# Optimization experiments

Hardware: AMD Instinct MI355X
Metric: run time of the kernel (lower is better)

Reference implementation:

```python
import jax, jax.numpy as jnp
import numpy as np

DIM = 768
N_HEADS = 12
HEAD_DIM = DIM // N_HEADS
MLP_DIM = 3072
DEPTH = 12
B, N = 16, 512


def setup_inputs() -> dict:
    key = jax.random.key(0)
    ks = jax.random.split(key, 12)
    s = 0.02
    return {
        "x": jax.random.normal(ks[0], (B, N, DIM), dtype=jnp.float32),
        "ln_w": jnp.ones((DIM,), jnp.float32),
        "ln_b": jnp.zeros((DIM,), jnp.float32),
        "wq": jax.random.normal(ks[1], (DIM, DIM), jnp.float32) * s,
        "bq": jnp.zeros((DIM,), jnp.float32),
        "wk": jax.random.normal(ks[2], (DIM, DIM), jnp.float32) * s,
        "bk": jnp.zeros((DIM,), jnp.float32),
        "wv": jax.random.normal(ks[3], (DIM, DIM), jnp.float32) * s,
        "bv": jnp.zeros((DIM,), jnp.float32),
        "w1": jax.random.normal(ks[4], (DIM, MLP_DIM), jnp.float32) * s,
        "b1": jnp.zeros((MLP_DIM,), jnp.float32),
        "w2": jax.random.normal(ks[5], (MLP_DIM, DIM), jnp.float32) * s,
        "b2": jnp.zeros((DIM,), jnp.float32),
    }


def _layernorm(x, w, b):
    mu = jnp.mean(x, axis=-1, keepdims=True)
    var = jnp.var(x, axis=-1, keepdims=True)
    return (x - mu) * jax.lax.rsqrt(var + 1e-5) * w + b


def _mha(x, wq, bq, wk, bk, wv, bv):
    # x: [b, n, dim]; weights stored as [in, out]
    def heads(t):
        return t.reshape(B, N, N_HEADS, HEAD_DIM).transpose(0, 2, 1, 3)  # b h n d
    q = heads(x @ wq + bq)
    k = heads(x @ wk + bk)
    v = heads(x @ wv + bv)
    scores = jnp.einsum('bhqd,bhkd->bhqk', q, k) / np.sqrt(HEAD_DIM).astype(np.float32)
    attn = jax.nn.softmax(scores, axis=-1)
    o = jnp.einsum('bhqk,bhkd->bhqd', attn, v)
    return o.transpose(0, 2, 1, 3).reshape(B, N, DIM)


def reference(x, ln_w, ln_b, wq, bq, wk, bk, wv, bv, w1, b1, w2, b2):
    # Dropout is identity in eval mode. Same weights reused each depth iteration.
    for _ in range(DEPTH):
        x = _mha(_layernorm(x, ln_w, ln_b), wq, bq, wk, bk, wv, bv) + x
        h = _layernorm(x, ln_w, ln_b)
        h = jax.nn.gelu(h @ w1 + b1, approximate=False) @ w2 + b2
        x = h + x
    return x
```

## Files before the change

### kernel.cpp

```cpp
#include <hip/hip_runtime.h>

typedef __bf16 bf16x8 __attribute__((ext_vector_type(8)));
typedef float f32x4 __attribute__((ext_vector_type(4)));
typedef unsigned short ushort8_t __attribute__((ext_vector_type(8)));
typedef unsigned short ushort4_t __attribute__((ext_vector_type(4)));

#define MFMA16(a, b, c) __builtin_amdgcn_mfma_f32_16x16x32_bf16((a), (b), (c), 0, 0, 0)

#define GLOAD16(gp, lp)                                                        \
  __builtin_amdgcn_global_load_lds(                                            \
      (__attribute__((address_space(1))) void*)(gp),                           \
      (__attribute__((address_space(3))) void*)(lp), 16, 0, 0)

__device__ __forceinline__ unsigned short f2bf(float f) {
  unsigned u = __builtin_bit_cast(unsigned, f);
  return (unsigned short)((u + 0x7FFFu + ((u >> 16) & 1u)) >> 16);
}

__global__ __launch_bounds__(256) void transpose_f2b(
    const float* __restrict__ src, unsigned short* __restrict__ dst,
    int Kdim, int Ndim) {
  long i = (long)blockIdx.x * 256 + threadIdx.x;
  if (i >= (long)Kdim * Ndim) return;
  int n = (int)(i / Kdim);
  int kk = (int)(i - (long)n * Kdim);
  dst[i] = f2bf(src[(long)kk * Ndim + n]);
}

__global__ __launch_bounds__(256) void ln_kernel(
    const float* __restrict__ x, const float* __restrict__ gw,
    const float* __restrict__ gb, unsigned short* __restrict__ h) {
  const int row = blockIdx.x * 4 + (threadIdx.x >> 6);
  const int l = threadIdx.x & 63;
  const float* xr = x + (long)row * 768;
  f32x4 va[3];
#pragma unroll
  for (int i = 0; i < 3; i++) va[i] = *(const f32x4*)(xr + i * 256 + l * 4);
  float s = 0.f, ss = 0.f;
#pragma unroll
  for (int i = 0; i < 3; i++)
#pragma unroll
    for (int j = 0; j < 4; j++) {
      float t = va[i][j];
      s += t;
      ss += t * t;
    }
#pragma unroll
  for (int off = 1; off < 64; off <<= 1) {
    s += __shfl_xor(s, off, 64);
    ss += __shfl_xor(ss, off, 64);
  }
  const float mu = s * (1.f / 768.f);
  const float var = ss * (1.f / 768.f) - mu * mu;
  const float inv = rsqrtf(var + 1e-5f);
  unsigned short* hp = h + (long)row * 768;
#pragma unroll
  for (int i = 0; i < 3; i++) {
    f32x4 wv = *(const f32x4*)(gw + i * 256 + l * 4);
    f32x4 bv = *(const f32x4*)(gb + i * 256 + l * 4);
    ushort4_t o;
#pragma unroll
    for (int j = 0; j < 4; j++) o[j] = f2bf((va[i][j] - mu) * inv * wv[j] + bv[j]);
    *(ushort4_t*)(hp + i * 256 + l * 4) = o;
  }
}

__global__ __launch_bounds__(256) void transpose_v(
    const unsigned short* __restrict__ v, unsigned short* __restrict__ vt) {
  __shared__ unsigned short t[64 * 65];
  const int n0 = blockIdx.x * 64;
  const int bh = blockIdx.y;
  const int tid = threadIdx.x;
  {
    const int n = tid >> 2, d0 = (tid & 3) * 16;
    const unsigned short* s = v + ((long)bh * 512 + n0 + n) * 64 + d0;
    ushort8_t r0 = *(const ushort8_t*)s;
    ushort8_t r1 = *(const ushort8_t*)(s + 8);
#pragma unroll
    for (int j = 0; j < 8; j++) {
      t[n * 65 + d0 + j] = r0[j];
      t[n * 65 + d0 + 8 + j] = r1[j];
    }
  }
  __syncthreads();
  {
    const int d = tid >> 2, nb = (tid & 3) * 16;
    ushort8_t r0, r1;
#pragma unroll
    for (int j = 0; j < 8; j++) {
      r0[j] = t[(nb + j) * 65 + d];
      r1[j] = t[(nb + 8 + j) * 65 + d];
    }
    unsigned short* o = vt + ((long)bh * 64 + d) * 512 + n0 + nb;
    *(ushort8_t*)o = r0;
    *(ushort8_t*)(o + 8) = r1;
  }
}

enum { EPI_QKV = 0, EPI_GELU = 1, EPI_RES = 2 };

template <int EPI, int MREP>
__global__ __launch_bounds__(256) void gemm_bt(
    const unsigned short* __restrict__ A, const unsigned short* __restrict__ BT,
    int K, const float* __restrict__ bb0, const float* __restrict__ bb1,
    const float* __restrict__ bb2, unsigned short* __restrict__ o0,
    unsigned short* __restrict__ o1, unsigned short* __restrict__ o2,
    float* oF) {
  constexpr int BM = MREP * 32;
  constexpr int ABUF = BM * 32;
  __shared__ unsigned short As[2][ABUF];
  __shared__ unsigned short Bs[2][128 * 32];
  const int tid = threadIdx.x;
  const int w = tid >> 6, l = tid & 63;
  const int lr = l & 15, lg = l >> 4;
  const int wr = w >> 1, wc = w & 1;

  const int nx = gridDim.x;
  const int nwg = nx * gridDim.y;
  int wg = blockIdx.y * nx + blockIdx.x;
  {
    const int qq = nwg >> 3, rr = nwg & 7;
    const int xcd = wg & 7, idx = wg >> 3;
    wg = (xcd < rr ? xcd * (qq + 1) : rr * (qq + 1) + (xcd - rr) * qq) + idx;
  }
  const int bx = wg % nx, by = wg / nx;
  const int m0 = by * BM, n0 = bx * 128;

  const unsigned short* Ag =
      A + (long)(m0 + w * (BM / 4) + (l >> 2)) * K + (l & 3) * 8;
  const unsigned short* Bg = BT + (long)(n0 + w * 32 + (l >> 2)) * K + (l & 3) * 8;
  unsigned short* AsW = &As[0][w * (BM / 4) * 32 + l * 8];
  unsigned short* BsW = &Bs[0][w * 1024 + l * 8];

  auto stage = [&](int buf, int kt) {
    const unsigned short* ag = Ag + kt * 32;
    const unsigned short* bg = Bg + kt * 32;
    unsigned short* aw = AsW + buf * ABUF;
    unsigned short* bw = BsW + buf * 4096;
#pragma unroll
    for (int i = 0; i < BM / 64; i++) GLOAD16(ag + i * 16 * K, aw + i * 512);
    GLOAD16(bg, bw);
    GLOAD16(bg + 16 * K, bw + 512);
  };

  f32x4 acc[MREP][4] = {};
  const int nk = K >> 5;
  stage(0, 0);
  __syncthreads();
  for (int kt = 0; kt < nk; ++kt) {
    const int cur = kt & 1;
    if (kt + 1 < nk) stage(cur ^ 1, kt + 1);
    const unsigned short* Ab = &As[cur][0];
    const unsigned short* Bb = &Bs[cur][0];
    bf16x8 a[MREP], b[4];
#pragma unroll
    for (int i = 0; i < MREP; i++)
      a[i] = *(const bf16x8*)(Ab + (wr * MREP * 16 + i * 16 + lr) * 32 + lg * 8);
#pragma unroll
    for (int j = 0; j < 4; j++)
      b[j] = *(const bf16x8*)(Bb + (wc * 64 + j * 16 + lr) * 32 + lg * 8);
#pragma unroll
    for (int i = 0; i < MREP; i++)
#pragma unroll
      for (int j = 0; j < 4; j++) acc[i][j] = MFMA16(a[i], b[j], acc[i][j]);
    __syncthreads();
  }

  if (EPI == EPI_QKV) {
    const int whichq = n0 / 768;
    const int cc0 = n0 - whichq * 768;
    const float* bias = whichq == 0 ? bb0 : whichq == 1 ? bb1 : bb2;
    unsigned short* dst = whichq == 0 ? o0 : whichq == 1 ? o1 : o2;
#pragma unroll
    for (int i = 0; i < MREP; i++) {
      const int r = m0 + wr * MREP * 16 + i * 16 + lg * 4;
#pragma unroll
      for (int j = 0; j < 4; j++) {
        const int ccol = cc0 + wc * 64 + j * 16 + lr;
        const int hd = ccol >> 6, d = ccol & 63;
        const float bv = bias[ccol];
#pragma unroll
        for (int q = 0; q < 4; q++) {
          const int row = r + q;
          const int bidx = row >> 9, n = row & 511;
          const long addr = ((long)(bidx * 12 + hd) * 512 + n) * 64 + d;
          dst[addr] = f2bf(acc[i][j][q] + bv);
        }
      }
    }
  } else if (EPI == EPI_GELU) {
#pragma unroll
    for (int i = 0; i < MREP; i++) {
      const int r = m0 + wr * MREP * 16 + i * 16 + lg * 4;
#pragma unroll
      for (int j = 0; j < 4; j++) {
        const int c = n0 + wc * 64 + j * 16 + lr;
        const float bv = bb0[c];
#pragma unroll
        for (int q = 0; q < 4; q++) {
          float v = acc[i][j][q] + bv;
          const float u = v * (0.7978845608f + 0.0356774081f * v * v);
          const float g = v / (1.0f + __expf(-2.0f * u));
          o0[(long)(r + q) * 3072 + c] = f2bf(g);
        }
      }
    }
  } else {
#pragma unroll
    for (int i = 0; i < MREP; i++) {
      const int r = m0 + wr * MREP * 16 + i * 16 + lg * 4;
#pragma unroll
      for (int j = 0; j < 4; j++) {
        const int c = n0 + wc * 64 + j * 16 + lr;
        const float bv = bb0[c];
#pragma unroll
        for (int q = 0; q < 4; q++) {
          const long addr = (long)(r + q) * 768 + c;
          oF[addr] = acc[i][j][q] + bv + oF[addr];
        }
      }
    }
  }
}

__global__ __launch_bounds__(256) void attn_kernel(
    const unsigned short* __restrict__ qg, const unsigned short* __restrict__ kg,
    const unsigned short* __restrict__ vtg, float* __restrict__ x) {
  __shared__ unsigned short Qs[128 * 64];
  __shared__ unsigned short Ks[2][64 * 64];
  __shared__ unsigned short Vt[2][64 * 64];
  __shared__ unsigned short Ps[4][32 * 64];
  const int qt = blockIdx.x, h = blockIdx.y, b = blockIdx.z;
  const int bh = b * 12 + h;
  const int tid = threadIdx.x, w = tid >> 6, l = tid & 63;
  const int lr = l & 15, lg = l >> 4;

  const unsigned short* qrow =
      qg + ((long)bh * 512 + qt * 128 + w * 32 + (l >> 3)) * 64 + (l & 7) * 8;
  unsigned short* QsW = &Qs[w * 2048 + l * 8];
#pragma unroll
  for (int cc = 0; cc < 4; cc++) GLOAD16(qrow + cc * 8 * 64, QsW + cc * 512);

  const unsigned short* krow =
      kg + ((long)bh * 512 + w * 16 + (l >> 3)) * 64 + (l & 7) * 8;
  const unsigned short* vrow =
      vtg + ((long)bh * 64 + w * 16 + (l >> 3)) * 512 + (l & 7) * 8;
  unsigned short* KsW = &Ks[0][w * 1024 + l * 8];
  unsigned short* VtW = &Vt[0][w * 1024 + l * 8];
  unsigned short* Pw = &Ps[w][0];

  auto stageKV = [&](int buf, int kt) {
#pragma unroll
    for (int cc = 0; cc < 2; cc++) {
      GLOAD16(krow + (kt * 64 + cc * 8) * 64, KsW + buf * 4096 + cc * 512);
      GLOAD16(vrow + cc * 8 * 512 + kt * 64, VtW + buf * 4096 + cc * 512);
    }
  };
  stageKV(0, 0);
  __syncthreads();

  bf16x8 qa[2][2];
#pragma unroll
  for (int mi = 0; mi < 2; mi++)
#pragma unroll
    for (int ds = 0; ds < 2; ds++) {
      qa[mi][ds] =
          *(const bf16x8*)(Qs + (w * 32 + mi * 16 + lr) * 64 + ds * 32 + lg * 8);
#pragma unroll
      for (int e = 0; e < 8; e++)
        qa[mi][ds][e] = (__bf16)(0.125f * (float)qa[mi][ds][e]);
    }

  float lsum[8] = {};
  f32x4 o[2][4] = {};

  for (int kt = 0; kt < 8; ++kt) {
    const int cur = kt & 1;
    if (kt < 7) stageKV(cur ^ 1, kt + 1);

    f32x4 s[2][4] = {};
#pragma unroll
    for (int ds = 0; ds < 2; ++ds) {
      bf16x8 kb[4];
#pragma unroll
      for (int nj = 0; nj < 4; nj++)
        kb[nj] = *(const bf16x8*)(&Ks[cur][0] + (nj * 16 + lr) * 64 + ds * 32 + lg * 8);
#pragma unroll
      for (int mi = 0; mi < 2; mi++)
#pragma unroll
        for (int nj = 0; nj < 4; nj++) s[mi][nj] = MFMA16(qa[mi][ds], kb[nj], s[mi][nj]);
    }

#pragma unroll
    for (int mi = 0; mi < 2; mi++)
#pragma unroll
      for (int nj = 0; nj < 4; nj++)
#pragma unroll
        for (int q = 0; q < 4; q++) {
          const float p = __expf(s[mi][nj][q]);
          lsum[mi * 4 + q] += p;
          Pw[(mi * 16 + lg * 4 + q) * 64 + nj * 16 + lr] = f2bf(p);
        }

#pragma unroll
    for (int ks = 0; ks < 2; ++ks) {
      bf16x8 pa[2], vb[4];
#pragma unroll
      for (int mi = 0; mi < 2; mi++)
        pa[mi] = *(const bf16x8*)(Pw + (mi * 16 + lr) * 64 + ks * 32 + lg * 8);
#pragma unroll
      for (int dj = 0; dj < 4; dj++)
        vb[dj] = *(const bf16x8*)(&Vt[cur][0] + (dj * 16 + lr) * 64 + ks * 32 + lg * 8);
#pragma unroll
      for (int mi = 0; mi < 2; mi++)
#pragma unroll
        for (int dj = 0; dj < 4; dj++) o[mi][dj] = MFMA16(pa[mi], vb[dj], o[mi][dj]);
    }
    __syncthreads();
  }

#pragma unroll
  for (int i = 0; i < 8; i++) {
#pragma unroll
    for (int off = 1; off < 16; off <<= 1) lsum[i] += __shfl_xor(lsum[i], off, 64);
  }

#pragma unroll
  for (int mi = 0; mi < 2; mi++) {
#pragma unroll
    for (int q = 0; q < 4; q++) {
      const int n = qt * 128 + w * 32 + mi * 16 + lg * 4 + q;
      const float inv = 1.0f / lsum[mi * 4 + q];
      const long base = ((long)(b * 512 + n)) * 768 + h * 64;
#pragma unroll
      for (int dj = 0; dj < 4; dj++) {
        const long a = base + dj * 16 + lr;
        x[a] = x[a] + o[mi][dj][q] * inv;
      }
    }
  }
}

extern "C" void kernel_launch(void* const* d_in, const int* in_sizes, int n_in,
                              void* d_out, int out_size, void* d_ws,
                              size_t ws_size, hipStream_t stream) {
  const float* x_in = (const float*)d_in[0];
  const float* ln_w = (const float*)d_in[1];
  const float* ln_b = (const float*)d_in[2];
  const float* wq = (const float*)d_in[3];
  const float* bq = (const float*)d_in[4];
  const float* wk = (const float*)d_in[5];
  const float* bk = (const float*)d_in[6];
  const float* wv = (const float*)d_in[7];
  const float* bv = (const float*)d_in[8];
  const float* w1 = (const float*)d_in[9];
  const float* b1 = (const float*)d_in[10];
  const float* w2 = (const float*)d_in[11];
  const float* b2 = (const float*)d_in[12];

  char* p = (char*)d_ws;
  float* xw = (float*)p;            p += 8192L * 768 * 4;
  unsigned short* hbuf = (unsigned short*)p;  p += 8192L * 768 * 2;
  unsigned short* wqkvT = (unsigned short*)p; p += 2304L * 768 * 2;
  unsigned short* w1T = (unsigned short*)p;   p += 3072L * 768 * 2;
  unsigned short* w2T = (unsigned short*)p;   p += 768L * 3072 * 2;
  unsigned short* qb = (unsigned short*)p;
  unsigned short* kb = qb + 6291456L;
  unsigned short* vb = kb + 6291456L;
  unsigned short* vt = vb + 6291456L;
  unsigned short* gbuf = qb;

  hipMemcpyAsync(xw, x_in, 8192L * 768 * 4, hipMemcpyDeviceToDevice, stream);

  transpose_f2b<<<(768 * 768 + 255) / 256, 256, 0, stream>>>(wq, wqkvT, 768, 768);
  transpose_f2b<<<(768 * 768 + 255) / 256, 256, 0, stream>>>(wk, wqkvT + 589824L, 768, 768);
  transpose_f2b<<<(768 * 768 + 255) / 256, 256, 0, stream>>>(wv, wqkvT + 1179648L, 768, 768);
  transpose_f2b<<<(768 * 3072 + 255) / 256, 256, 0, stream>>>(w1, w1T, 768, 3072);
  transpose_f2b<<<(768 * 3072 + 255) / 256, 256, 0, stream>>>(w2, w2T, 3072, 768);

  for (int layer = 0; layer < 12; ++layer) {
    ln_kernel<<<2048, 256, 0, stream>>>(xw, ln_w, ln_b, hbuf);
    gemm_bt<EPI_QKV, 4><<<dim3(18, 64), 256, 0, stream>>>(
        hbuf, wqkvT, 768, bq, bk, bv, qb, kb, vb, nullptr);
    transpose_v<<<dim3(8, 192), 256, 0, stream>>>(vb, vt);
    attn_kernel<<<dim3(4, 12, 16), 256, 0, stream>>>(qb, kb, vt, xw);
    ln_kernel<<<2048, 256, 0, stream>>>(xw, ln_w, ln_b, hbuf);
    gemm_bt<EPI_GELU, 4><<<dim3(24, 64), 256, 0, stream>>>(
        hbuf, w1T, 768, b1, nullptr, nullptr, gbuf, nullptr, nullptr, nullptr);
    gemm_bt<EPI_RES, 2><<<dim3(6, 128), 256, 0, stream>>>(
        gbuf, w2T, 3072, b2, nullptr, nullptr, nullptr, nullptr, nullptr, xw);
  }

  hipMemcpyAsync(d_out, xw, 8192L * 768 * 4, hipMemcpyDeviceToDevice, stream);
}
```

Baseline: 2.856 ms.

## Swizzle LDS tiles, write V transposed in QKV epilogue, drop final copy

Applies an XOR swizzle to the global-to-LDS chunk placement and the matching fragment reads in both the GEMM and attention kernels, to remove LDS bank conflicts. The QKV GEMM epilogue now writes V directly in transposed layout, which removes the separate transpose_v kernel and its extra read and write of V. Attention reuses the Q shared buffer for the P tile, cutting LDS usage and possibly raising occupancy. The last MLP residual GEMM writes straight to the output, which removes the final device-to-device copy. The swizzle indexing must match exactly between the load and read sides, and the transposed V stores are 8-byte scattered writes.

```diff
diff --git a/kernel.cpp b/kernel.cpp
--- a/kernel.cpp
+++ b/kernel.cpp
@@ -65,38 +65,6 @@
   }
 }
 
-__global__ __launch_bounds__(256) void transpose_v(
-    const unsigned short* __restrict__ v, unsigned short* __restrict__ vt) {
-  __shared__ unsigned short t[64 * 65];
-  const int n0 = blockIdx.x * 64;
-  const int bh = blockIdx.y;
-  const int tid = threadIdx.x;
-  {
-    const int n = tid >> 2, d0 = (tid & 3) * 16;
-    const unsigned short* s = v + ((long)bh * 512 + n0 + n) * 64 + d0;
-    ushort8_t r0 = *(const ushort8_t*)s;
-    ushort8_t r1 = *(const ushort8_t*)(s + 8);
-#pragma unroll
-    for (int j = 0; j < 8; j++) {
-      t[n * 65 + d0 + j] = r0[j];
-      t[n * 65 + d0 + 8 + j] = r1[j];
-    }
-  }
-  __syncthreads();
-  {
-    const int d = tid >> 2, nb = (tid & 3) * 16;
-    ushort8_t r0, r1;
-#pragma unroll
-    for (int j = 0; j < 8; j++) {
-      r0[j] = t[(nb + j) * 65 + d];
-      r1[j] = t[(nb + 8 + j) * 65 + d];
-    }
-    unsigned short* o = vt + ((long)bh * 64 + d) * 512 + n0 + nb;
-    *(ushort8_t*)o = r0;
-    *(ushort8_t*)(o + 8) = r1;
-  }
-}
-
 enum { EPI_QKV = 0, EPI_GELU = 1, EPI_RES = 2 };
 
 template <int EPI, int MREP>
@@ -105,7 +73,7 @@
     int K, const float* __restrict__ bb0, const float* __restrict__ bb1,
     const float* __restrict__ bb2, unsigned short* __restrict__ o0,
     unsigned short* __restrict__ o1, unsigned short* __restrict__ o2,
-    float* oF) {
+    const float* oFin, float* oFout) {
   constexpr int BM = MREP * 32;
   constexpr int ABUF = BM * 32;
   __shared__ unsigned short As[2][ABUF];
@@ -114,6 +82,8 @@
   const int w = tid >> 6, l = tid & 63;
   const int lr = l & 15, lg = l >> 4;
   const int wr = w >> 1, wc = w & 1;
+  const int fchunk = ((l & 3) ^ ((l >> 3) & 3)) * 8;
+  const int sR = (lr >> 1) & 3;
 
   const int nx = gridDim.x;
   const int nwg = nx * gridDim.y;
@@ -127,8 +97,8 @@
   const int m0 = by * BM, n0 = bx * 128;
 
   const unsigned short* Ag =
-      A + (long)(m0 + w * (BM / 4) + (l >> 2)) * K + (l & 3) * 8;
-  const unsigned short* Bg = BT + (long)(n0 + w * 32 + (l >> 2)) * K + (l & 3) * 8;
+      A + (long)(m0 + w * (BM / 4) + (l >> 2)) * K + fchunk;
+  const unsigned short* Bg = BT + (long)(n0 + w * 32 + (l >> 2)) * K + fchunk;
   unsigned short* AsW = &As[0][w * (BM / 4) * 32 + l * 8];
   unsigned short* BsW = &Bs[0][w * 1024 + l * 8];
 
@@ -150,15 +120,15 @@
   for (int kt = 0; kt < nk; ++kt) {
     const int cur = kt & 1;
     if (kt + 1 < nk) stage(cur ^ 1, kt + 1);
-    const unsigned short* Ab = &As[cur][0];
-    const unsigned short* Bb = &Bs[cur][0];
     bf16x8 a[MREP], b[4];
 #pragma unroll
     for (int i = 0; i < MREP; i++)
-      a[i] = *(const bf16x8*)(Ab + (wr * MREP * 16 + i * 16 + lr) * 32 + lg * 8);
+      a[i] = *(const bf16x8*)(&As[cur][(wr * MREP * 16 + i * 16 + lr) * 32 +
+                                       ((lg ^ sR) * 8)]);
 #pragma unroll
     for (int j = 0; j < 4; j++)
-      b[j] = *(const bf16x8*)(Bb + (wc * 64 + j * 16 + lr) * 32 + lg * 8);
+      b[j] = *(const bf16x8*)(&Bs[cur][(wc * 64 + j * 16 + lr) * 32 +
+                                       ((lg ^ sR) * 8)]);
 #pragma unroll
     for (int i = 0; i < MREP; i++)
 #pragma unroll
@@ -170,21 +140,39 @@
     const int whichq = n0 / 768;
     const int cc0 = n0 - whichq * 768;
     const float* bias = whichq == 0 ? bb0 : whichq == 1 ? bb1 : bb2;
-    unsigned short* dst = whichq == 0 ? o0 : whichq == 1 ? o1 : o2;
-#pragma unroll
-    for (int i = 0; i < MREP; i++) {
-      const int r = m0 + wr * MREP * 16 + i * 16 + lg * 4;
-#pragma unroll
-      for (int j = 0; j < 4; j++) {
-        const int ccol = cc0 + wc * 64 + j * 16 + lr;
-        const int hd = ccol >> 6, d = ccol & 63;
-        const float bv = bias[ccol];
-#pragma unroll
-        for (int q = 0; q < 4; q++) {
-          const int row = r + q;
-          const int bidx = row >> 9, n = row & 511;
-          const long addr = ((long)(bidx * 12 + hd) * 512 + n) * 64 + d;
-          dst[addr] = f2bf(acc[i][j][q] + bv);
+    if (whichq < 2) {
+      unsigned short* dst = whichq == 0 ? o0 : o1;
+#pragma unroll
+      for (int i = 0; i < MREP; i++) {
+        const int r = m0 + wr * MREP * 16 + i * 16 + lg * 4;
+#pragma unroll
+        for (int j = 0; j < 4; j++) {
+          const int ccol = cc0 + wc * 64 + j * 16 + lr;
+          const int hd = ccol >> 6, d = ccol & 63;
+          const float bv = bias[ccol];
+#pragma unroll
+          for (int q = 0; q < 4; q++) {
+            const int row = r + q;
+            const int bidx = row >> 9, n = row & 511;
+            const long addr = ((long)(bidx * 12 + hd) * 512 + n) * 64 + d;
+            dst[addr] = f2bf(acc[i][j][q] + bv);
+          }
+        }
+      }
+    } else {
+#pragma unroll
+      for (int i = 0; i < MREP; i++) {
+        const int r = m0 + wr * MREP * 16 + i * 16 + lg * 4;
+        const int bidx = r >> 9, n = r & 511;
+#pragma unroll
+        for (int j = 0; j < 4; j++) {
+          const int ccol = cc0 + wc * 64 + j * 16 + lr;
+          const int hd = ccol >> 6, d = ccol & 63;
+          const float bv = bias[ccol];
+          ushort4_t pk;
+#pragma unroll
+          for (int q = 0; q < 4; q++) pk[q] = f2bf(acc[i][j][q] + bv);
+          *(ushort4_t*)(&o2[((long)(bidx * 12 + hd) * 64 + d) * 512 + n]) = pk;
         }
       }
     }
@@ -216,7 +204,7 @@
 #pragma unroll
         for (int q = 0; q < 4; q++) {
           const long addr = (long)(r + q) * 768 + c;
-          oF[addr] = acc[i][j][q] + bv + oF[addr];
+          oFout[addr] = acc[i][j][q] + bv + oFin[addr];
         }
       }
     }
@@ -226,34 +214,34 @@
 __global__ __launch_bounds__(256) void attn_kernel(
     const unsigned short* __restrict__ qg, const unsigned short* __restrict__ kg,
     const unsigned short* __restrict__ vtg, float* __restrict__ x) {
-  __shared__ unsigned short Qs[128 * 64];
+  __shared__ unsigned short Sh[128 * 64];
   __shared__ unsigned short Ks[2][64 * 64];
   __shared__ unsigned short Vt[2][64 * 64];
-  __shared__ unsigned short Ps[4][32 * 64];
   const int qt = blockIdx.x, h = blockIdx.y, b = blockIdx.z;
   const int bh = b * 12 + h;
   const int tid = threadIdx.x, w = tid >> 6, l = tid & 63;
   const int lr = l & 15, lg = l >> 4;
-
-  const unsigned short* qrow =
-      qg + ((long)bh * 512 + qt * 128 + w * 32 + (l >> 3)) * 64 + (l & 7) * 8;
-  unsigned short* QsW = &Qs[w * 2048 + l * 8];
-#pragma unroll
-  for (int cc = 0; cc < 4; cc++) GLOAD16(qrow + cc * 8 * 64, QsW + cc * 512);
-
-  const unsigned short* krow =
-      kg + ((long)bh * 512 + w * 16 + (l >> 3)) * 64 + (l & 7) * 8;
-  const unsigned short* vrow =
-      vtg + ((long)bh * 64 + w * 16 + (l >> 3)) * 512 + (l & 7) * 8;
+  const int fchunk = ((l & 7) ^ ((l >> 3) & 7)) * 8;
+  const int rk = lr & 7;
+
+  const unsigned short* qbase =
+      qg + ((long)bh * 512 + qt * 128 + w * 32 + (l >> 3)) * 64 + fchunk;
+  unsigned short* shW = &Sh[w * 2048 + l * 8];
+#pragma unroll
+  for (int cc = 0; cc < 4; cc++) GLOAD16(qbase + cc * 8 * 64, shW + cc * 512);
+
+  const unsigned short* kbase =
+      kg + ((long)bh * 512 + w * 16 + (l >> 3)) * 64 + fchunk;
+  const unsigned short* vbase =
+      vtg + ((long)bh * 64 + w * 16 + (l >> 3)) * 512 + fchunk;
   unsigned short* KsW = &Ks[0][w * 1024 + l * 8];
   unsigned short* VtW = &Vt[0][w * 1024 + l * 8];
-  unsigned short* Pw = &Ps[w][0];
 
   auto stageKV = [&](int buf, int kt) {
 #pragma unroll
     for (int cc = 0; cc < 2; cc++) {
-      GLOAD16(krow + (kt * 64 + cc * 8) * 64, KsW + buf * 4096 + cc * 512);
-      GLOAD16(vrow + cc * 8 * 512 + kt * 64, VtW + buf * 4096 + cc * 512);
+      GLOAD16(kbase + (kt * 64 + cc * 8) * 64, KsW + buf * 4096 + cc * 512);
+      GLOAD16(vbase + cc * 8 * 512 + kt * 64, VtW + buf * 4096 + cc * 512);
     }
   };
   stageKV(0, 0);
@@ -264,13 +252,14 @@
   for (int mi = 0; mi < 2; mi++)
 #pragma unroll
     for (int ds = 0; ds < 2; ds++) {
-      qa[mi][ds] =
-          *(const bf16x8*)(Qs + (w * 32 + mi * 16 + lr) * 64 + ds * 32 + lg * 8);
+      qa[mi][ds] = *(const bf16x8*)(&Sh[(w * 32 + mi * 16 + lr) * 64 +
+                                        ((ds * 4 + lg) ^ rk) * 8]);
 #pragma unroll
       for (int e = 0; e < 8; e++)
         qa[mi][ds][e] = (__bf16)(0.125f * (float)qa[mi][ds][e]);
     }
 
+  unsigned short* Pw = &Sh[w * 2048];
   float lsum[8] = {};
   f32x4 o[2][4] = {};
 
@@ -284,7 +273,8 @@
       bf16x8 kb[4];
 #pragma unroll
       for (int nj = 0; nj < 4; nj++)
-        kb[nj] = *(const bf16x8*)(&Ks[cur][0] + (nj * 16 + lr) * 64 + ds * 32 + lg * 8);
+        kb[nj] = *(const bf16x8*)(&Ks[cur][(nj * 16 + lr) * 64 +
+                                           ((ds * 4 + lg) ^ rk) * 8]);
 #pragma unroll
       for (int mi = 0; mi < 2; mi++)
 #pragma unroll
@@ -294,23 +284,28 @@
 #pragma unroll
     for (int mi = 0; mi < 2; mi++)
 #pragma unroll
-      for (int nj = 0; nj < 4; nj++)
+      for (int nj = 0; nj < 4; nj++) {
+        const int cL = nj * 2 + (lr >> 3);
 #pragma unroll
         for (int q = 0; q < 4; q++) {
+          const int row = mi * 16 + lg * 4 + q;
           const float p = __expf(s[mi][nj][q]);
           lsum[mi * 4 + q] += p;
-          Pw[(mi * 16 + lg * 4 + q) * 64 + nj * 16 + lr] = f2bf(p);
-        }
+          Pw[row * 64 + ((cL ^ (row & 7)) * 8) + (lr & 7)] = f2bf(p);
+        }
+      }
 
 #pragma unroll
     for (int ks = 0; ks < 2; ++ks) {
       bf16x8 pa[2], vb[4];
 #pragma unroll
       for (int mi = 0; mi < 2; mi++)
-        pa[mi] = *(const bf16x8*)(Pw + (mi * 16 + lr) * 64 + ks * 32 + lg * 8);
+        pa[mi] = *(const bf16x8*)(&Pw[(mi * 16 + lr) * 64 +
+                                      ((ks * 4 + lg) ^ rk) * 8]);
 #pragma unroll
       for (int dj = 0; dj < 4; dj++)
-        vb[dj] = *(const bf16x8*)(&Vt[cur][0] + (dj * 16 + lr) * 64 + ks * 32 + lg * 8);
+        vb[dj] = *(const bf16x8*)(&Vt[cur][(dj * 16 + lr) * 64 +
+                                           ((ks * 4 + lg) ^ rk) * 8]);
 #pragma unroll
       for (int mi = 0; mi < 2; mi++)
 #pragma unroll
@@ -366,8 +361,7 @@
   unsigned short* w2T = (unsigned short*)p;   p += 768L * 3072 * 2;
   unsigned short* qb = (unsigned short*)p;
   unsigned short* kb = qb + 6291456L;
-  unsigned short* vb = kb + 6291456L;
-  unsigned short* vt = vb + 6291456L;
+  unsigned short* vt = kb + 6291456L;
   unsigned short* gbuf = qb;
 
   hipMemcpyAsync(xw, x_in, 8192L * 768 * 4, hipMemcpyDeviceToDevice, stream);
@@ -381,15 +375,14 @@
   for (int layer = 0; layer < 12; ++layer) {
     ln_kernel<<<2048, 256, 0, stream>>>(xw, ln_w, ln_b, hbuf);
     gemm_bt<EPI_QKV, 4><<<dim3(18, 64), 256, 0, stream>>>(
-        hbuf, wqkvT, 768, bq, bk, bv, qb, kb, vb, nullptr);
-    transpose_v<<<dim3(8, 192), 256, 0, stream>>>(vb, vt);
+        hbuf, wqkvT, 768, bq, bk, bv, qb, kb, vt, nullptr, nullptr);
     attn_kernel<<<dim3(4, 12, 16), 256, 0, stream>>>(qb, kb, vt, xw);
     ln_kernel<<<2048, 256, 0, stream>>>(xw, ln_w, ln_b, hbuf);
     gemm_bt<EPI_GELU, 4><<<dim3(24, 64), 256, 0, stream>>>(
-        hbuf, w1T, 768, b1, nullptr, nullptr, gbuf, nullptr, nullptr, nullptr);
+        hbuf, w1T, 768, b1, nullptr, nullptr, gbuf, nullptr, nullptr, nullptr,
+        nullptr);
     gemm_bt<EPI_RES, 2><<<dim3(6, 128), 256, 0, stream>>>(
-        gbuf, w2T, 3072, b2, nullptr, nullptr, nullptr, nullptr, nullptr, xw);
-  }
-
-  hipMemcpyAsync(d_out, xw, 8192L * 768 * 4, hipMemcpyDeviceToDevice, stream);
-}
+        gbuf, w2T, 3072, b2, nullptr, nullptr, nullptr, nullptr, nullptr, xw,
+        layer == 11 ? (float*)d_out : xw);
+  }
+}
```

After: 2.888 ms. No clear change (+1.1%).
